# Kernel tuning notes

Hardware: AMD Instinct MI355X
Metric: run time of the kernel (lower is better)

Reference implementation:

```python
import jax, jax.numpy as jnp
import numpy as np

I_T = 0.5       # IoU threshold self.I_t
GAMMA = 2.0     # focal loss gamma
EPS = 1e-7      # focal loss eps clamp
BS, P, C_IN = 8, 2048, 512


def pairwise_iou(b):
    # b: (bs, P, 4) xyxy -> (bs, P, P), same math as torchvision box_iou (no +1)
    area = (b[..., 2] - b[..., 0]) * (b[..., 3] - b[..., 1])
    lt = jnp.maximum(b[:, :, None, :2], b[:, None, :, :2])
    rb = jnp.minimum(b[:, :, None, 2:], b[:, None, :, 2:])
    wh = jnp.clip(rb - lt, 0.0, None)
    inter = wh[..., 0] * wh[..., 1]
    return inter / (area[:, :, None] + area[:, None, :] - inter)


def assign_labels_weights(pre_score, labels, rois):
    # Vectorized, order-faithful version of the per-batch/per-class python loop.
    # Selected seeds per class c: proposals with pre_score[...,c] > 0.5 if more than
    # one, else the single argmax proposal (torch code falls back when k<=1).
    # Sequential `_I > old` running max over (c, j) in ascending order is equivalent
    # to a global first-occurrence argmax (strict >), so per-class max + running
    # compare with earlier-class tie preference reproduces it exactly.
    bs, Pn = pre_score.shape[0], pre_score.shape[1]
    iou = pairwise_iou(rois)                      # (bs, P, P)
    run_I = jnp.full((bs, Pn), -1.0, pre_score.dtype)
    run_w = jnp.ones((bs, Pn), pre_score.dtype)
    hits = []
    for c in range(3):
        s = pre_score[:, :, c]                    # (bs, P)
        th = s > 0.5
        cnt = th.sum(-1)
        onehot = jnp.arange(Pn)[None, :] == jnp.argmax(s, -1)[:, None]
        sel = jnp.where((cnt > 1)[:, None], th, onehot)
        sel = sel & (labels[:, c] != 0)[:, None]  # skip classes absent from image
        masked = jnp.where(sel[:, None, :], iou, -2.0)  # (bs, P, P)
        val = masked.max(-1)                      # best IoU vs any seed of class c
        jidx = masked.argmax(-1)
        cand_x = jnp.take_along_axis(s, jidx, axis=1)
        better = val > run_I
        run_w = jnp.where(better, cand_x, run_w)
        run_I = jnp.where(better, val, run_I)
        hits.append(val > I_T)
    hit = jnp.stack(hits, -1)                     # (bs, P, 3)
    bg = (~hit.any(-1))[..., None]
    y = jnp.concatenate([hit.astype(pre_score.dtype), bg.astype(pre_score.dtype)], -1)
    return y, run_w


def icr_forward(inputs, fc_w, fc_b, pre_score, labels, rois, num):
    bs = inputs.shape[0] // num
    xr = inputs @ fc_w + fc_b                     # (bs*P, 4)
    logit = jax.nn.softmax(xr.reshape(bs, num, 4), -1)
    ps = jax.lax.stop_gradient(pre_score)         # .clone().detach()
    lb = jax.lax.stop_gradient(labels)
    y, w = assign_labels_weights(ps, lb, rois)
    y = y.reshape(bs * num, 4)
    w = w.reshape(bs * num, 1)
    # FocalLoss(gamma=2, mode='none')
    p = jnp.clip(jax.nn.softmax(xr, -1), EPS, 1.0 - EPS)
    fl = -y * jnp.log(p) * (1.0 - p) ** GAMMA
    imbalance = y.sum(0)                          # (4,)
    loss = (w * fl / (imbalance + 1e-7)).reshape(bs, num, 4)
    lab = lb.at[:, 3].set(1.0)[:, None, :]        # lab[:,0,3]=1
    w_ = 10.0 * jnp.exp(logit) * (1.0 - lab) + lab
    loss = (loss * w_).sum() / bs
    return logit, loss


def setup_inputs():
    key = jax.random.key(0)
    k = jax.random.split(key, 6)
    inputs = jax.random.normal(k[0], (BS * P, C_IN), jnp.float32)
    fc_w = jax.random.normal(k[1], (C_IN, 4), jnp.float32) * 0.02
    fc_b = jnp.zeros((4,), jnp.float32)
    pre_score = jax.random.uniform(k[2], (BS, P, 4), dtype=jnp.float32)
    labels = (jax.random.uniform(k[3], (BS, 4)) < 0.5).astype(jnp.float32)
    labels = labels.at[:, 3].set(0.0)
    xy = jax.random.uniform(k[4], (BS, P, 2), dtype=jnp.float32) * 448.0
    wh = jax.random.uniform(k[5], (BS, P, 2), dtype=jnp.float32) * 63.0 + 1.0
    rois = jnp.concatenate([xy, xy + wh], -1)     # valid xyxy boxes in 512x512
    return {"inputs": inputs, "fc_w": fc_w, "fc_b": fc_b, "pre_score": pre_score,
            "labels": labels, "rois": rois, "num": P}


def reference(inputs, fc_w, fc_b, pre_score, labels, rois, num):
    return icr_forward(inputs, fc_w, fc_b, pre_score, labels, rois, num)
```

## Files before the change

kernel.cpp:

```cpp
#include <hip/hip_runtime.h>

#define BSZ 8
#define PN  2048
#define CIN 512
#define CAP 2048
#define NW  16


__global__ __launch_bounds__(256) void k_sel(
    const float* __restrict__ ps, const float* __restrict__ labels,
    const float* __restrict__ rois, float* __restrict__ accum,
    int* __restrict__ meta, float* __restrict__ sList,
    float* __restrict__ areaL, float4* __restrict__ roiList)
{
  const int t  = threadIdx.x;
  const int bc = blockIdx.x;
  if (bc == 0 && t < 12) accum[t] = 0.0f;
  const int b = bc / 3;
  const int c = bc % 3;
  const int j0 = t * 8;

  float sv[8];
  int   flg = 0, cnt = 0;
  float vmax = -1e30f;
  int   jmax = 0;
  #pragma unroll
  for (int m = 0; m < 8; ++m) {
    const float s = ps[(b * PN + j0 + m) * 4 + c];
    sv[m] = s;
    if (s > 0.5f) { flg |= 1 << m; ++cnt; }
    if (s > vmax) { vmax = s; jmax = j0 + m; }
  }

  __shared__ float lv[256];
  __shared__ int   lj[256];
  __shared__ int   pre[256];
  lv[t] = vmax; lj[t] = jmax; pre[t] = cnt;
  __syncthreads();
  for (int off = 128; off > 0; off >>= 1) {
    if (t < off) {
      const float v2 = lv[t + off]; const int j2 = lj[t + off];
      if (v2 > lv[t] || (v2 == lv[t] && j2 < lj[t])) { lv[t] = v2; lj[t] = j2; }
    }
    __syncthreads();
  }
  for (int off = 1; off < 256; off <<= 1) {
    const int add = (t >= off) ? pre[t - off] : 0;
    __syncthreads();
    pre[t] += add;
    __syncthreads();
  }
  const int  totalTh = pre[255];
  const int  excl    = pre[t] - cnt;
  const int  jArg    = lj[0];
  const bool lab     = labels[b * 4 + c] != 0.0f;
  const int  L    = (!lab) ? 0 : ((totalTh > 1) ? totalTh : 1);
  const int  Lpad = (L + 7) & ~7;

  __shared__ float4 lastRoi;
  __shared__ float  lastS, lastA;
  float4* dstR = roiList + bc * CAP;
  float*  dstS = sList   + bc * CAP;
  float*  dstA = areaL   + bc * CAP;
  const float4* rb = ((const float4*)rois) + b * PN;

  if (lab) {
    if (totalTh > 1) {
      int pos = excl;
      #pragma unroll
      for (int m = 0; m < 8; ++m) {
        if (flg & (1 << m)) {
          const float4 r = rb[j0 + m];
          const float  a = (r.z - r.x) * (r.w - r.y);
          dstR[pos] = r; dstS[pos] = sv[m]; dstA[pos] = a;
          if (pos == L - 1) { lastRoi = r; lastS = sv[m]; lastA = a; }
          ++pos;
        }
      }
    } else if (t == (jArg >> 3)) {
      const float4 r = rb[jArg];
      const float  a = (r.z - r.x) * (r.w - r.y);
      dstR[0] = r; dstS[0] = sv[jArg & 7]; dstA[0] = a;
      lastRoi = r; lastS = sv[jArg & 7]; lastA = a;
    }
  }
  __syncthreads();
  if (t < Lpad - L) { dstR[L + t] = lastRoi; dstS[L + t] = lastS; dstA[L + t] = lastA; }
  if (t == 0) meta[bc] = Lpad;
}

__global__ __launch_bounds__(1024, 8) void k_fused(
    const float* __restrict__ inp, const float* __restrict__ fcw,
    const float* __restrict__ fcb, const float* __restrict__ rois,
    const int* __restrict__ meta, const float4* __restrict__ roiList,
    const float* __restrict__ areaL, float* __restrict__ logit,
    float* __restrict__ pbn, float* __restrict__ pbd, int* __restrict__ pbp)
{
  const int t    = threadIdx.x;
  const int lane = t & 63;
  const int wv   = t >> 6;

  __shared__ __align__(16) char ldsraw[61440];

  if (blockIdx.x >= 256) {
    const int gw = ((int)blockIdx.x - 256) * NW + wv;
    const int kb = lane << 2;
    const float4 wa0 = *(const float4*)(fcw + (kb + 0) * 4);
    const float4 wa1 = *(const float4*)(fcw + (kb + 1) * 4);
    const float4 wa2 = *(const float4*)(fcw + (kb + 2) * 4);
    const float4 wa3 = *(const float4*)(fcw + (kb + 3) * 4);
    const float4 wb0 = *(const float4*)(fcw + (256 + kb + 0) * 4);
    const float4 wb1 = *(const float4*)(fcw + (256 + kb + 1) * 4);
    const float4 wb2 = *(const float4*)(fcw + (256 + kb + 2) * 4);
    const float4 wb3 = *(const float4*)(fcw + (256 + kb + 3) * 4);
    const float4 bias = *(const float4*)fcb;
    #pragma unroll
    for (int rr = 0; rr < 4; ++rr) {
      const int r = (gw << 2) + rr;
      const float* row = inp + r * CIN;
      const float4 xa = *(const float4*)(row + kb);
      const float4 xb = *(const float4*)(row + 256 + kb);
      float a0 = xa.x*wa0.x + xa.y*wa1.x + xa.z*wa2.x + xa.w*wa3.x
               + xb.x*wb0.x + xb.y*wb1.x + xb.z*wb2.x + xb.w*wb3.x;
      float a1 = xa.x*wa0.y + xa.y*wa1.y + xa.z*wa2.y + xa.w*wa3.y
               + xb.x*wb0.y + xb.y*wb1.y + xb.z*wb2.y + xb.w*wb3.y;
      float a2 = xa.x*wa0.z + xa.y*wa1.z + xa.z*wa2.z + xa.w*wa3.z
               + xb.x*wb0.z + xb.y*wb1.z + xb.z*wb2.z + xb.w*wb3.z;
      float a3 = xa.x*wa0.w + xa.y*wa1.w + xa.z*wa2.w + xa.w*wa3.w
               + xb.x*wb0.w + xb.y*wb1.w + xb.z*wb2.w + xb.w*wb3.w;
      #pragma unroll
      for (int off = 32; off; off >>= 1) {
        a0 += __shfl_xor(a0, off); a1 += __shfl_xor(a1, off);
        a2 += __shfl_xor(a2, off); a3 += __shfl_xor(a3, off);
      }
      if (lane == 0) {
        a0 += bias.x; a1 += bias.y; a2 += bias.z; a3 += bias.w;
        const float m  = fmaxf(fmaxf(a0, a1), fmaxf(a2, a3));
        const float e0 = expf(a0 - m), e1 = expf(a1 - m);
        const float e2 = expf(a2 - m), e3 = expf(a3 - m);
        const float inv = 1.0f / (e0 + e1 + e2 + e3);
        float4 o; o.x = e0*inv; o.y = e1*inv; o.z = e2*inv; o.w = e3*inv;
        *(float4*)(logit + r * 4) = o;
      }
    }
    return;
  }

  const int blk = blockIdx.x;
  const int h   = blk & 1;
  const int it  = (blk >> 1) & 15;
  const int b   = blk >> 5;

  float4* sroi  = (float4*)ldsraw;
  float*  sarea = (float*)(ldsraw + 49152);
  float*  mn    = (float*)ldsraw;
  float*  md    = (float*)(ldsraw + 12288);
  int*    mp    = (int*)(ldsraw + 24576);

  int startc[3], cntc[3];
  #pragma unroll
  for (int c = 0; c < 3; ++c) {
    const int L  = meta[b * 3 + c];
    const int L2 = ((L >> 1) + 7) & ~7;
    const int s0 = h ? L2 : 0;
    const int e0 = h ? L  : L2;
    startc[c] = s0;
    cntc[c]   = e0 - s0;
    if (t < cntc[c]) {
      sroi [c * 1024 + t] = roiList[(b * 3 + c) * CAP + s0 + t];
      sarea[c * 1024 + t] = areaL  [(b * 3 + c) * CAP + s0 + t];
    }
  }
  const int i0 = (it << 7) + lane;
  const float4 ri0 = ((const float4*)rois)[b * PN + i0];
  const float4 ri1 = ((const float4*)rois)[b * PN + i0 + 64];
  const float ar0 = (ri0.z - ri0.x) * (ri0.w - ri0.y);
  const float ar1 = (ri1.z - ri1.x) * (ri1.w - ri1.y);
  __syncthreads();

  auto upd = [](const float4 ri, const float ai,
                float& n, float& d, int& p,
                const float4 rj, const float aj, const int pos) {
    const float lx = fmaxf(ri.x, rj.x), ly = fmaxf(ri.y, rj.y);
    const float rx = fminf(ri.z, rj.z), ry = fminf(ri.w, rj.w);
    const float ww = fmaxf(rx - lx, 0.0f), hh = fmaxf(ry - ly, 0.0f);
    const float inter = ww * hh;
    const float uni   = ai + aj - inter;
    if (inter * d > n * uni) { n = inter; d = uni; p = pos; }
  };

  float BN[3][2], BD[3][2]; int BP[3][2];
  #pragma unroll
  for (int c = 0; c < 3; ++c) {
    const int cnt = cntc[c];
    const int C   = (((cnt + 15) >> 4) + 7) & ~7;
    const int g0  = wv * C;
    int g1 = g0 + C; if (g1 > cnt) g1 = cnt;
    const float4* rbase = sroi  + c * 1024;
    const float*  abase = sarea + c * 1024;
    float n0A = -2.0f, d0A = 1.0f, n0B = -2.0f, d0B = 1.0f;
    float n1A = -2.0f, d1A = 1.0f, n1B = -2.0f, d1B = 1.0f;
    int   p0A = 0, p0B = 0, p1A = 0, p1B = 0;

    for (int g = g0; g < g1; g += 2) {
      const float4 r0_ = rbase[g], r1_ = rbase[g + 1];
      const float  a0_ = abase[g], a1_ = abase[g + 1];
      upd(ri0, ar0, n0A, d0A, p0A, r0_, a0_, g);
      upd(ri1, ar1, n1A, d1A, p1A, r0_, a0_, g);
      upd(ri0, ar0, n0B, d0B, p0B, r1_, a1_, g + 1);
      upd(ri1, ar1, n1B, d1B, p1B, r1_, a1_, g + 1);
    }
    {
      const float tB = n0B * d0A, tA = n0A * d0B;
      if (tB > tA || (tB == tA && p0B < p0A)) { n0A = n0B; d0A = d0B; p0A = p0B; }
    }
    {
      const float tB = n1B * d1A, tA = n1A * d1B;
      if (tB > tA || (tB == tA && p1B < p1A)) { n1A = n1B; d1A = d1B; p1A = p1B; }
    }
    BN[c][0] = n0A; BD[c][0] = d0A; BP[c][0] = p0A + startc[c];
    BN[c][1] = n1A; BD[c][1] = d1A; BP[c][1] = p1A + startc[c];
  }
  __syncthreads();
  #pragma unroll
  for (int ii = 0; ii < 2; ++ii) {
    #pragma unroll
    for (int c = 0; c < 3; ++c) {
      mn[(c * NW + wv) * 64 + lane] = BN[c][ii];
      md[(c * NW + wv) * 64 + lane] = BD[c][ii];
      mp[(c * NW + wv) * 64 + lane] = BP[c][ii];
    }
    __syncthreads();
    if (wv == 0) {
      #pragma unroll
      for (int c = 0; c < 3; ++c) {
        float bn = BN[c][ii], bd = BD[c][ii]; int bp = BP[c][ii];
        for (int w2 = 1; w2 < NW; ++w2) {
          const float n = mn[(c * NW + w2) * 64 + lane];
          const float d = md[(c * NW + w2) * 64 + lane];
          const int   p = mp[(c * NW + w2) * 64 + lane];
          if (n * bd > bn * d) { bn = n; bd = d; bp = p; }
        }
        const int ig = (it << 7) + (ii << 6) + lane;
        const int o  = ((b * 3 + c) * 2 + h) * PN + ig;
        pbn[o] = bn; pbd[o] = bd; pbp[o] = bp;
      }
    }
    __syncthreads();
  }
}

__global__ __launch_bounds__(256) void k_back(
    const float* __restrict__ pbn, const float* __restrict__ pbd,
    const int* __restrict__ pbp, const float* __restrict__ sList,
    const float* __restrict__ logit, const float* __restrict__ labels,
    float* __restrict__ accum, float* __restrict__ loss)
{
  const int t  = threadIdx.x;
  const int gi = blockIdx.x * 256 + t;
  const int b  = gi >> 11;
  const int i  = gi & (PN - 1);

  float v[3], sc[3];
  #pragma unroll
  for (int c = 0; c < 3; ++c) {
    const int o0 = ((b * 3 + c) * 2) * PN + i;
    float n = pbn[o0], d = pbd[o0]; int p = pbp[o0];
    const float n1 = pbn[o0 + PN], d1 = pbd[o0 + PN];
    const int   p1 = pbp[o0 + PN];
    if (n1 * d > n * d1) { n = n1; d = d1; p = p1; }
    v[c]  = n / d;
    sc[c] = sList[(b * 3 + c) * CAP + p];
  }
  float runI = -1.0f, runw = 1.0f;
  if (v[0] > runI) { runw = sc[0]; runI = v[0]; }
  if (v[1] > runI) { runw = sc[1]; runI = v[1]; }
  if (v[2] > runI) { runw = sc[2]; runI = v[2]; }
  const float y0 = (v[0] > 0.5f) ? 1.0f : 0.0f;
  const float y1 = (v[1] > 0.5f) ? 1.0f : 0.0f;
  const float y2 = (v[2] > 0.5f) ? 1.0f : 0.0f;
  const float y3 = (y0 + y1 + y2 == 0.0f) ? 1.0f : 0.0f;

  const float4 lg = ((const float4*)logit)[gi];
  const float lb0 = labels[b * 4 + 0];
  const float lb1 = labels[b * 4 + 1];
  const float lb2 = labels[b * 4 + 2];

  auto term = [&](const float l, const float yv, const float labv) -> float {
    const float p  = fminf(fmaxf(l, 1e-7f), 1.0f - 1e-7f);
    const float om = 1.0f - p;
    const float fl = -yv * logf(p) * om * om;
    const float wl = 10.0f * expf(l) * (1.0f - labv) + labv;
    return runw * fl * wl;
  };
  float s[8];
  s[0] = term(lg.x, y0, lb0); s[1] = term(lg.y, y1, lb1);
  s[2] = term(lg.z, y2, lb2); s[3] = term(lg.w, y3, 1.0f);
  s[4] = y0; s[5] = y1; s[6] = y2; s[7] = y3;

  #pragma unroll
  for (int k = 0; k < 8; ++k)
    #pragma unroll
    for (int off = 32; off; off >>= 1) s[k] += __shfl_xor(s[k], off);

  __shared__ float red[4][8];
  const int wv = t >> 6;
  if ((t & 63) == 0)
    #pragma unroll
    for (int k = 0; k < 8; ++k) red[wv][k] = s[k];
  __syncthreads();
  if (t < 8) {
    const float sum = red[0][t] + red[1][t] + red[2][t] + red[3][t];
    atomicAdd(&accum[t], sum);
  }
  __syncthreads();
  if (t == 0) {
    __threadfence();
    const int ticket = __hip_atomic_fetch_add((int*)(accum + 8), 1,
                        __ATOMIC_ACQ_REL, __HIP_MEMORY_SCOPE_AGENT);
    if (ticket == 63) {
      float L = 0.0f;
      #pragma unroll
      for (int c = 0; c < 4; ++c) {
        const float num = __hip_atomic_load(accum + c,
                            __ATOMIC_RELAXED, __HIP_MEMORY_SCOPE_AGENT);
        const float den = __hip_atomic_load(accum + 4 + c,
                            __ATOMIC_RELAXED, __HIP_MEMORY_SCOPE_AGENT);
        L += num / (den + 1e-7f);
      }
      loss[0] = L * 0.125f;
    }
  }
}

extern "C" void kernel_launch(void* const* d_in, const int* in_sizes, int n_in,
                              void* d_out, int out_size, void* d_ws, size_t ws_size,
                              hipStream_t stream)
{
  (void)in_sizes; (void)n_in; (void)out_size; (void)ws_size;
  const float* inp    = (const float*)d_in[0];
  const float* fcw    = (const float*)d_in[1];
  const float* fcb    = (const float*)d_in[2];
  const float* ps     = (const float*)d_in[3];
  const float* labels = (const float*)d_in[4];
  const float* rois   = (const float*)d_in[5];
  float* out = (float*)d_out;

  char* ws = (char*)d_ws;
  float*  accum   = (float*) (ws);
  int*    meta    = (int*)   (ws + 64);
  float*  sList   = (float*) (ws + 1024);
  float*  areaL   = (float*) (ws + 197632);
  float4* roiL    = (float4*)(ws + 394240);
  float*  pbn     = (float*) (ws + 1180672);
  float*  pbd     = (float*) (ws + 1573888);
  int*    pbp     = (int*)   (ws + 1967104);

  k_sel  <<<24,  256,  0, stream>>>(ps, labels, rois, accum, meta, sList, areaL, roiL);
  k_fused<<<512, 1024, 0, stream>>>(inp, fcw, fcb, rois, meta, roiL, areaL,
                                    out, pbn, pbd, pbp);
  k_back <<<64,  256,  0, stream>>>(pbn, pbd, pbp, sList, out, labels, accum,
                                    out + BSZ * PN * 4);
}
```

Measured before the change: 123.7 us.

## Split FC/softmax across selection and IoU kernels, recompute areas in IoU loop

Part of the FC+softmax rows (12288 of 16384) now runs inside the selection kernel as extra blocks, so that short kernel does useful work alongside the per-class selection. The remaining 4096 rows run in half the warps of the IoU kernel, while the other 8 warps do the pairwise IoU search. The IoU kernel drops to 256 blocks, each doing more IoU work per warp. The area list is no longer stored; areas are recomputed from the roi in the inner loop, which removes one LDS array and global buffer at the cost of extra ALU per pair.

```diff
diff --git a/kernel.cpp b/kernel.cpp
--- a/kernel.cpp
+++ b/kernel.cpp
@@ -4,107 +4,21 @@
 #define PN  2048
 #define CIN 512
 #define CAP 2048
-#define NW  16
-
-
-__global__ __launch_bounds__(256) void k_sel(
-    const float* __restrict__ ps, const float* __restrict__ labels,
-    const float* __restrict__ rois, float* __restrict__ accum,
+
+
+__global__ __launch_bounds__(256) void k_front(
+    const float* __restrict__ inp, const float* __restrict__ fcw,
+    const float* __restrict__ fcb, const float* __restrict__ ps,
+    const float* __restrict__ labels, const float* __restrict__ rois,
+    float* __restrict__ logit, float* __restrict__ accum,
     int* __restrict__ meta, float* __restrict__ sList,
-    float* __restrict__ areaL, float4* __restrict__ roiList)
+    float4* __restrict__ roiList)
 {
-  const int t  = threadIdx.x;
-  const int bc = blockIdx.x;
-  if (bc == 0 && t < 12) accum[t] = 0.0f;
-  const int b = bc / 3;
-  const int c = bc % 3;
-  const int j0 = t * 8;
-
-  float sv[8];
-  int   flg = 0, cnt = 0;
-  float vmax = -1e30f;
-  int   jmax = 0;
-  #pragma unroll
-  for (int m = 0; m < 8; ++m) {
-    const float s = ps[(b * PN + j0 + m) * 4 + c];
-    sv[m] = s;
-    if (s > 0.5f) { flg |= 1 << m; ++cnt; }
-    if (s > vmax) { vmax = s; jmax = j0 + m; }
-  }
-
-  __shared__ float lv[256];
-  __shared__ int   lj[256];
-  __shared__ int   pre[256];
-  lv[t] = vmax; lj[t] = jmax; pre[t] = cnt;
-  __syncthreads();
-  for (int off = 128; off > 0; off >>= 1) {
-    if (t < off) {
-      const float v2 = lv[t + off]; const int j2 = lj[t + off];
-      if (v2 > lv[t] || (v2 == lv[t] && j2 < lj[t])) { lv[t] = v2; lj[t] = j2; }
-    }
-    __syncthreads();
-  }
-  for (int off = 1; off < 256; off <<= 1) {
-    const int add = (t >= off) ? pre[t - off] : 0;
-    __syncthreads();
-    pre[t] += add;
-    __syncthreads();
-  }
-  const int  totalTh = pre[255];
-  const int  excl    = pre[t] - cnt;
-  const int  jArg    = lj[0];
-  const bool lab     = labels[b * 4 + c] != 0.0f;
-  const int  L    = (!lab) ? 0 : ((totalTh > 1) ? totalTh : 1);
-  const int  Lpad = (L + 7) & ~7;
-
-  __shared__ float4 lastRoi;
-  __shared__ float  lastS, lastA;
-  float4* dstR = roiList + bc * CAP;
-  float*  dstS = sList   + bc * CAP;
-  float*  dstA = areaL   + bc * CAP;
-  const float4* rb = ((const float4*)rois) + b * PN;
-
-  if (lab) {
-    if (totalTh > 1) {
-      int pos = excl;
-      #pragma unroll
-      for (int m = 0; m < 8; ++m) {
-        if (flg & (1 << m)) {
-          const float4 r = rb[j0 + m];
-          const float  a = (r.z - r.x) * (r.w - r.y);
-          dstR[pos] = r; dstS[pos] = sv[m]; dstA[pos] = a;
-          if (pos == L - 1) { lastRoi = r; lastS = sv[m]; lastA = a; }
-          ++pos;
-        }
-      }
-    } else if (t == (jArg >> 3)) {
-      const float4 r = rb[jArg];
-      const float  a = (r.z - r.x) * (r.w - r.y);
-      dstR[0] = r; dstS[0] = sv[jArg & 7]; dstA[0] = a;
-      lastRoi = r; lastS = sv[jArg & 7]; lastA = a;
-    }
-  }
-  __syncthreads();
-  if (t < Lpad - L) { dstR[L + t] = lastRoi; dstS[L + t] = lastS; dstA[L + t] = lastA; }
-  if (t == 0) meta[bc] = Lpad;
-}
-
-__global__ __launch_bounds__(1024, 8) void k_fused(
-    const float* __restrict__ inp, const float* __restrict__ fcw,
-    const float* __restrict__ fcb, const float* __restrict__ rois,
-    const int* __restrict__ meta, const float4* __restrict__ roiList,
-    const float* __restrict__ areaL, float* __restrict__ logit,
-    float* __restrict__ pbn, float* __restrict__ pbd, int* __restrict__ pbp)
-{
-  const int t    = threadIdx.x;
-  const int lane = t & 63;
-  const int wv   = t >> 6;
-
-  __shared__ __align__(16) char ldsraw[61440];
-
-  if (blockIdx.x >= 256) {
-    const int gw = ((int)blockIdx.x - 256) * NW + wv;
-    const int kb = lane << 2;
+  const int t = threadIdx.x;
+  if (blockIdx.x >= 24) {
+    const int gw   = (((int)blockIdx.x - 24) * 256 + t) >> 6;
+    const int lane = t & 63;
+    const int kb   = lane << 2;
     const float4 wa0 = *(const float4*)(fcw + (kb + 0) * 4);
     const float4 wa1 = *(const float4*)(fcw + (kb + 1) * 4);
     const float4 wa2 = *(const float4*)(fcw + (kb + 2) * 4);
@@ -146,16 +60,98 @@
     return;
   }
 
-  const int blk = blockIdx.x;
-  const int h   = blk & 1;
-  const int it  = (blk >> 1) & 15;
-  const int b   = blk >> 5;
-
-  float4* sroi  = (float4*)ldsraw;
-  float*  sarea = (float*)(ldsraw + 49152);
-  float*  mn    = (float*)ldsraw;
-  float*  md    = (float*)(ldsraw + 12288);
-  int*    mp    = (int*)(ldsraw + 24576);
+  const int bc = blockIdx.x;
+  if (bc == 0 && t < 12) accum[t] = 0.0f;
+  const int b = bc / 3;
+  const int c = bc % 3;
+  const int j0 = t * 8;
+
+  float sv[8];
+  int   flg = 0, cnt = 0;
+  float vmax = -1e30f;
+  int   jmax = 0;
+  #pragma unroll
+  for (int m = 0; m < 8; ++m) {
+    const float s = ps[(b * PN + j0 + m) * 4 + c];
+    sv[m] = s;
+    if (s > 0.5f) { flg |= 1 << m; ++cnt; }
+    if (s > vmax) { vmax = s; jmax = j0 + m; }
+  }
+
+  __shared__ float lv[256];
+  __shared__ int   lj[256];
+  __shared__ int   pre[256];
+  lv[t] = vmax; lj[t] = jmax; pre[t] = cnt;
+  __syncthreads();
+  for (int off = 128; off > 0; off >>= 1) {
+    if (t < off) {
+      const float v2 = lv[t + off]; const int j2 = lj[t + off];
+      if (v2 > lv[t] || (v2 == lv[t] && j2 < lj[t])) { lv[t] = v2; lj[t] = j2; }
+    }
+    __syncthreads();
+  }
+  for (int off = 1; off < 256; off <<= 1) {
+    const int add = (t >= off) ? pre[t - off] : 0;
+    __syncthreads();
+    pre[t] += add;
+    __syncthreads();
+  }
+  const int  totalTh = pre[255];
+  const int  excl    = pre[t] - cnt;
+  const int  jArg    = lj[0];
+  const bool lab     = labels[b * 4 + c] != 0.0f;
+  const int  L    = (!lab) ? 0 : ((totalTh > 1) ? totalTh : 1);
+  const int  Lpad = (L + 7) & ~7;
+
+  __shared__ float4 lastRoi;
+  __shared__ float  lastS;
+  float4* dstR = roiList + bc * CAP;
+  float*  dstS = sList   + bc * CAP;
+  const float4* rb = ((const float4*)rois) + b * PN;
+
+  if (lab) {
+    if (totalTh > 1) {
+      int pos = excl;
+      #pragma unroll
+      for (int m = 0; m < 8; ++m) {
+        if (flg & (1 << m)) {
+          const float4 r = rb[j0 + m];
+          dstR[pos] = r; dstS[pos] = sv[m];
+          if (pos == L - 1) { lastRoi = r; lastS = sv[m]; }
+          ++pos;
+        }
+      }
+    } else if (t == (jArg >> 3)) {
+      const float4 r = rb[jArg];
+      dstR[0] = r; dstS[0] = sv[jArg & 7];
+      lastRoi = r; lastS = sv[jArg & 7];
+    }
+  }
+  __syncthreads();
+  if (t < Lpad - L) { dstR[L + t] = lastRoi; dstS[L + t] = lastS; }
+  if (t == 0) meta[bc] = Lpad;
+}
+
+__global__ __launch_bounds__(1024, 4) void k_mid(
+    const float* __restrict__ inp, const float* __restrict__ fcw,
+    const float* __restrict__ fcb, const float* __restrict__ rois,
+    const int* __restrict__ meta, const float4* __restrict__ roiList,
+    float* __restrict__ logit,
+    float* __restrict__ pbn, float* __restrict__ pbd, int* __restrict__ pbp)
+{
+  const int blk  = blockIdx.x;
+  const int t    = threadIdx.x;
+  const int lane = t & 63;
+  const int wv   = t >> 6;
+
+  const int b  = blk >> 5;
+  const int h  = (blk >> 4) & 1;
+  const int it = blk & 15;
+
+  __shared__ __align__(16) float4 sroi[3 * 1024];
+  float* mn = (float*)sroi;
+  float* md = (float*)sroi + 1536;
+  int*   mp = (int*)((float*)sroi + 3072);
 
   int startc[3], cntc[3];
   #pragma unroll
@@ -166,79 +162,125 @@
     const int e0 = h ? L  : L2;
     startc[c] = s0;
     cntc[c]   = e0 - s0;
-    if (t < cntc[c]) {
-      sroi [c * 1024 + t] = roiList[(b * 3 + c) * CAP + s0 + t];
-      sarea[c * 1024 + t] = areaL  [(b * 3 + c) * CAP + s0 + t];
-    }
-  }
-  const int i0 = (it << 7) + lane;
-  const float4 ri0 = ((const float4*)rois)[b * PN + i0];
-  const float4 ri1 = ((const float4*)rois)[b * PN + i0 + 64];
-  const float ar0 = (ri0.z - ri0.x) * (ri0.w - ri0.y);
-  const float ar1 = (ri1.z - ri1.x) * (ri1.w - ri1.y);
-  __syncthreads();
-
-  auto upd = [](const float4 ri, const float ai,
-                float& n, float& d, int& p,
-                const float4 rj, const float aj, const int pos) {
-    const float lx = fmaxf(ri.x, rj.x), ly = fmaxf(ri.y, rj.y);
-    const float rx = fminf(ri.z, rj.z), ry = fminf(ri.w, rj.w);
-    const float ww = fmaxf(rx - lx, 0.0f), hh = fmaxf(ry - ly, 0.0f);
-    const float inter = ww * hh;
-    const float uni   = ai + aj - inter;
-    if (inter * d > n * uni) { n = inter; d = uni; p = pos; }
-  };
+    if (t < cntc[c])
+      sroi[c * 1024 + t] = roiList[(b * 3 + c) * CAP + s0 + t];
+  }
+  __syncthreads();
 
   float BN[3][2], BD[3][2]; int BP[3][2];
-  #pragma unroll
-  for (int c = 0; c < 3; ++c) {
-    const int cnt = cntc[c];
-    const int C   = (((cnt + 15) >> 4) + 7) & ~7;
-    const int g0  = wv * C;
-    int g1 = g0 + C; if (g1 > cnt) g1 = cnt;
-    const float4* rbase = sroi  + c * 1024;
-    const float*  abase = sarea + c * 1024;
-    float n0A = -2.0f, d0A = 1.0f, n0B = -2.0f, d0B = 1.0f;
-    float n1A = -2.0f, d1A = 1.0f, n1B = -2.0f, d1B = 1.0f;
-    int   p0A = 0, p0B = 0, p1A = 0, p1B = 0;
-
-    for (int g = g0; g < g1; g += 2) {
-      const float4 r0_ = rbase[g], r1_ = rbase[g + 1];
-      const float  a0_ = abase[g], a1_ = abase[g + 1];
-      upd(ri0, ar0, n0A, d0A, p0A, r0_, a0_, g);
-      upd(ri1, ar1, n1A, d1A, p1A, r0_, a0_, g);
-      upd(ri0, ar0, n0B, d0B, p0B, r1_, a1_, g + 1);
-      upd(ri1, ar1, n1B, d1B, p1B, r1_, a1_, g + 1);
-    }
-    {
-      const float tB = n0B * d0A, tA = n0A * d0B;
-      if (tB > tA || (tB == tA && p0B < p0A)) { n0A = n0B; d0A = d0B; p0A = p0B; }
-    }
-    {
-      const float tB = n1B * d1A, tA = n1A * d1B;
-      if (tB > tA || (tB == tA && p1B < p1A)) { n1A = n1B; d1A = d1B; p1A = p1B; }
-    }
-    BN[c][0] = n0A; BD[c][0] = d0A; BP[c][0] = p0A + startc[c];
-    BN[c][1] = n1A; BD[c][1] = d1A; BP[c][1] = p1A + startc[c];
-  }
+
+  if (wv < 8) {
+    const int i0 = (it << 7) + lane;
+    const float4 ri0 = ((const float4*)rois)[b * PN + i0];
+    const float4 ri1 = ((const float4*)rois)[b * PN + i0 + 64];
+    const float ar0 = (ri0.z - ri0.x) * (ri0.w - ri0.y);
+    const float ar1 = (ri1.z - ri1.x) * (ri1.w - ri1.y);
+
+    auto upd = [](const float4 ri, const float ai,
+                  float& n, float& d, int& p,
+                  const float4 rj, const float aj, const int pos) {
+      const float lx = fmaxf(ri.x, rj.x), ly = fmaxf(ri.y, rj.y);
+      const float rx = fminf(ri.z, rj.z), ry = fminf(ri.w, rj.w);
+      const float ww = fmaxf(rx - lx, 0.0f), hh = fmaxf(ry - ly, 0.0f);
+      const float inter = ww * hh;
+      const float uni   = ai + aj - inter;
+      if (inter * d > n * uni) { n = inter; d = uni; p = pos; }
+    };
+
+    #pragma unroll
+    for (int c = 0; c < 3; ++c) {
+      const int cnt = cntc[c];
+      const int C   = (((cnt + 7) >> 3) + 7) & ~7;
+      const int g0  = wv * C;
+      int g1 = g0 + C; if (g1 > cnt) g1 = cnt;
+      const float4* rbase = sroi + c * 1024;
+      float n0A = -2.0f, d0A = 1.0f, n0B = -2.0f, d0B = 1.0f;
+      float n1A = -2.0f, d1A = 1.0f, n1B = -2.0f, d1B = 1.0f;
+      int   p0A = 0, p0B = 0, p1A = 0, p1B = 0;
+
+      for (int g = g0; g < g1; g += 2) {
+        const float4 r0_ = rbase[g], r1_ = rbase[g + 1];
+        const float  a0_ = (r0_.z - r0_.x) * (r0_.w - r0_.y);
+        const float  a1_ = (r1_.z - r1_.x) * (r1_.w - r1_.y);
+        upd(ri0, ar0, n0A, d0A, p0A, r0_, a0_, g);
+        upd(ri1, ar1, n1A, d1A, p1A, r0_, a0_, g);
+        upd(ri0, ar0, n0B, d0B, p0B, r1_, a1_, g + 1);
+        upd(ri1, ar1, n1B, d1B, p1B, r1_, a1_, g + 1);
+      }
+      {
+        const float tB = n0B * d0A, tA = n0A * d0B;
+        if (tB > tA || (tB == tA && p0B < p0A)) { n0A = n0B; d0A = d0B; p0A = p0B; }
+      }
+      {
+        const float tB = n1B * d1A, tA = n1A * d1B;
+        if (tB > tA || (tB == tA && p1B < p1A)) { n1A = n1B; d1A = d1B; p1A = p1B; }
+      }
+      BN[c][0] = n0A; BD[c][0] = d0A; BP[c][0] = p0A + startc[c];
+      BN[c][1] = n1A; BD[c][1] = d1A; BP[c][1] = p1A + startc[c];
+    }
+  } else {
+    const int fw = (blk << 3) + (wv - 8);
+    const int kb = lane << 2;
+    const float4 wa0 = *(const float4*)(fcw + (kb + 0) * 4);
+    const float4 wa1 = *(const float4*)(fcw + (kb + 1) * 4);
+    const float4 wa2 = *(const float4*)(fcw + (kb + 2) * 4);
+    const float4 wa3 = *(const float4*)(fcw + (kb + 3) * 4);
+    const float4 wb0 = *(const float4*)(fcw + (256 + kb + 0) * 4);
+    const float4 wb1 = *(const float4*)(fcw + (256 + kb + 1) * 4);
+    const float4 wb2 = *(const float4*)(fcw + (256 + kb + 2) * 4);
+    const float4 wb3 = *(const float4*)(fcw + (256 + kb + 3) * 4);
+    const float4 bias = *(const float4*)fcb;
+    #pragma unroll
+    for (int rr = 0; rr < 2; ++rr) {
+      const int r = 12288 + (fw << 1) + rr;
+      const float* row = inp + r * CIN;
+      const float4 xa = *(const float4*)(row + kb);
+      const float4 xb = *(const float4*)(row + 256 + kb);
+      float a0 = xa.x*wa0.x + xa.y*wa1.x + xa.z*wa2.x + xa.w*wa3.x
+               + xb.x*wb0.x + xb.y*wb1.x + xb.z*wb2.x + xb.w*wb3.x;
+      float a1 = xa.x*wa0.y + xa.y*wa1.y + xa.z*wa2.y + xa.w*wa3.y
+               + xb.x*wb0.y + xb.y*wb1.y + xb.z*wb2.y + xb.w*wb3.y;
+      float a2 = xa.x*wa0.z + xa.y*wa1.z + xa.z*wa2.z + xa.w*wa3.z
+               + xb.x*wb0.z + xb.y*wb1.z + xb.z*wb2.z + xb.w*wb3.z;
+      float a3 = xa.x*wa0.w + xa.y*wa1.w + xa.z*wa2.w + xa.w*wa3.w
+               + xb.x*wb0.w + xb.y*wb1.w + xb.z*wb2.w + xb.w*wb3.w;
+      #pragma unroll
+      for (int off = 32; off; off >>= 1) {
+        a0 += __shfl_xor(a0, off); a1 += __shfl_xor(a1, off);
+        a2 += __shfl_xor(a2, off); a3 += __shfl_xor(a3, off);
+      }
+      if (lane == 0) {
+        a0 += bias.x; a1 += bias.y; a2 += bias.z; a3 += bias.w;
+        const float m  = fmaxf(fmaxf(a0, a1), fmaxf(a2, a3));
+        const float e0 = expf(a0 - m), e1 = expf(a1 - m);
+        const float e2 = expf(a2 - m), e3 = expf(a3 - m);
+        const float inv = 1.0f / (e0 + e1 + e2 + e3);
+        float4 o; o.x = e0*inv; o.y = e1*inv; o.z = e2*inv; o.w = e3*inv;
+        *(float4*)(logit + r * 4) = o;
+      }
+    }
+  }
+
   __syncthreads();
   #pragma unroll
   for (int ii = 0; ii < 2; ++ii) {
-    #pragma unroll
-    for (int c = 0; c < 3; ++c) {
-      mn[(c * NW + wv) * 64 + lane] = BN[c][ii];
-      md[(c * NW + wv) * 64 + lane] = BD[c][ii];
-      mp[(c * NW + wv) * 64 + lane] = BP[c][ii];
+    if (wv < 8) {
+      #pragma unroll
+      for (int c = 0; c < 3; ++c) {
+        mn[(c * 8 + wv) * 64 + lane] = BN[c][ii];
+        md[(c * 8 + wv) * 64 + lane] = BD[c][ii];
+        mp[(c * 8 + wv) * 64 + lane] = BP[c][ii];
+      }
     }
     __syncthreads();
     if (wv == 0) {
       #pragma unroll
       for (int c = 0; c < 3; ++c) {
         float bn = BN[c][ii], bd = BD[c][ii]; int bp = BP[c][ii];
-        for (int w2 = 1; w2 < NW; ++w2) {
-          const float n = mn[(c * NW + w2) * 64 + lane];
-          const float d = md[(c * NW + w2) * 64 + lane];
-          const int   p = mp[(c * NW + w2) * 64 + lane];
+        for (int w2 = 1; w2 < 8; ++w2) {
+          const float n = mn[(c * 8 + w2) * 64 + lane];
+          const float d = md[(c * 8 + w2) * 64 + lane];
+          const int   p = mp[(c * 8 + w2) * 64 + lane];
           if (n * bd > bn * d) { bn = n; bd = d; bp = p; }
         }
         const int ig = (it << 7) + (ii << 6) + lane;
@@ -350,14 +392,14 @@
   float*  accum   = (float*) (ws);
   int*    meta    = (int*)   (ws + 64);
   float*  sList   = (float*) (ws + 1024);
-  float*  areaL   = (float*) (ws + 197632);
   float4* roiL    = (float4*)(ws + 394240);
   float*  pbn     = (float*) (ws + 1180672);
   float*  pbd     = (float*) (ws + 1573888);
   int*    pbp     = (int*)   (ws + 1967104);
 
-  k_sel  <<<24,  256,  0, stream>>>(ps, labels, rois, accum, meta, sList, areaL, roiL);
-  k_fused<<<512, 1024, 0, stream>>>(inp, fcw, fcb, rois, meta, roiL, areaL,
+  k_front<<<792, 256,  0, stream>>>(inp, fcw, fcb, ps, labels, rois,
+                                    out, accum, meta, sList, roiL);
+  k_mid  <<<256, 1024, 0, stream>>>(inp, fcw, fcb, rois, meta, roiL,
                                     out, pbn, pbd, pbp);
   k_back <<<64,  256,  0, stream>>>(pbn, pbd, pbp, sList, out, labels, accum,
                                     out + BSZ * PN * 4);
```

After: 120.6 us. 1.03x faster.
